# Performance work log

Hardware: AMD Instinct MI355X
Metric: run time of the kernel (lower is better)

## Reference

```python
import jax, jax.numpy as jnp
import numpy as np

B, T, H, L = 128, 256, 512, 2  # batch, seq_len, hidden(=input), num_layers


def setup_inputs() -> dict:
    key = jax.random.key(0)
    k0, k1, k2, k3 = jax.random.split(key, 4)
    s = 1.0 / np.sqrt(H)  # torch Linear default init range
    x = jax.random.normal(k0, (B, T, H), jnp.float32)
    # Gate order along last dim: [i, f, g, o]; axis 1 = direction (0=fwd, 1=bwd)
    Wx = jax.random.uniform(k1, (L, 2, H, 4 * H), jnp.float32, -s, s)  # input->gates (W_ii,W_if,W_ig,W_io)
    Wh = jax.random.uniform(k2, (L, 2, H, 4 * H), jnp.float32, -s, s)  # hidden->gates (no bias)
    b = jax.random.uniform(k3, (L, 2, 4 * H), jnp.float32, -s, s)      # input-projection biases
    return {"x": x, "Wx": Wx, "Wh": Wh, "b": b}


def _lstm_scan(xproj, Wh_ld):
    # xproj: [T, B, 4H] precomputed input projection; Wh_ld: [H, 4H]
    Hh = Wh_ld.shape[0]
    bsz = xproj.shape[1]
    h0 = jnp.zeros((bsz, Hh), xproj.dtype)
    c0 = jnp.zeros((bsz, Hh), xproj.dtype)

    def step(carry, xp):
        h, c = carry
        gates = xp + h @ Wh_ld  # [B, 4H]
        i = jax.nn.sigmoid(gates[:, :Hh])
        f = jax.nn.sigmoid(gates[:, Hh:2 * Hh])
        g = jnp.tanh(gates[:, 2 * Hh:3 * Hh])
        o = jax.nn.sigmoid(gates[:, 3 * Hh:])
        c_new = f * c + i * g
        h_new = o * jnp.tanh(c_new)
        return (h_new, c_new), h_new

    _, hs = jax.lax.scan(step, (h0, c0), xproj)
    return hs  # [T, B, H]


def _run_direction(x, Wx, Wh, b, d):
    # x: [B, T, in]; d=0 forward, d=1 backward (time-reversed)
    nl = Wx.shape[0]
    seq = jnp.flip(x, axis=1) if d == 1 else x
    inp = seq
    for l in range(nl):
        # batched input projection over all timesteps (one big GEMM)
        xproj = jnp.einsum('bti,ig->btg', inp, Wx[l, d]) + b[l, d]  # [B, T, 4H]
        hs = _lstm_scan(jnp.transpose(xproj, (1, 0, 2)), Wh[l, d])   # [T, B, H]
        inp = jnp.transpose(hs, (1, 0, 2))  # [B, T, H]
        # dropout between layers is identity at inference
    return jnp.flip(inp, axis=1) if d == 1 else inp


def reference(x, Wx, Wh, b):
    fwd = _run_direction(x, Wx, Wh, b, 0)
    bwd = _run_direction(x, Wx, Wh, b, 1)
    return jnp.concatenate([fwd, bwd], axis=-1)  # [B, T, 2H]
```

## Files before the change

kernel.cpp:

```cpp
#include <hip/hip_runtime.h>

typedef unsigned short ushort_t;
typedef unsigned int u32;
typedef unsigned long long u64;
typedef __attribute__((ext_vector_type(8))) short short8;
typedef __attribute__((ext_vector_type(4))) float floatx4;

#define Tt 256
#define Hh 512
#define NBLK 256
#define THREADS 512
#define RWS 64
#define PING_ELEMS 65536u
#define KCH 256
#define SLOT_SHORTS (RWS * KCH)
#define SMEM_BYTES (2*SLOT_SHORTS*2 + RWS*16*2 + RWS*16*4)

__device__ __forceinline__ float sigf(float x)  { return 1.0f / (1.0f + __expf(-x)); }
__device__ __forceinline__ float tanhf_(float x){ return 1.0f - 2.0f / (__expf(2.0f*x) + 1.0f); }

__device__ __forceinline__ ushort_t f2bf(float f) {
  u32 u = __float_as_uint(f);
  u += 0x7FFFu + ((u >> 16) & 1u);
  return (ushort_t)(u >> 16);
}

__device__ __forceinline__ u64 pload(const ushort_t* p) {
  return __hip_atomic_load((const u64*)p, __ATOMIC_RELAXED, __HIP_MEMORY_SCOPE_AGENT);
}
__device__ __forceinline__ void pstore(ushort_t* p, u64 v) {
  __hip_atomic_store((u64*)p, v, __ATOMIC_RELAXED, __HIP_MEMORY_SCOPE_AGENT);
}
__device__ __forceinline__ u32 aload32(const u32* p) {
  return __hip_atomic_load(p, __ATOMIC_RELAXED, __HIP_MEMORY_SCOPE_AGENT);
}
__device__ __forceinline__ void astore32(u32* p, u32 v) {
  __hip_atomic_store(p, v, __ATOMIC_RELAXED, __HIP_MEMORY_SCOPE_AGENT);
}

__device__ __forceinline__ void gridbar(u32* gen, u32* flags, int fi, bool agg,
                                        u32 target) {
  __syncthreads();
  const int tid = threadIdx.x;
  if (agg) {
    if (tid < 64) {
      if (tid == 0) {
        asm volatile("s_waitcnt vmcnt(0)" ::: "memory");
        astore32(flags + fi * 16, target);
      }
      for (;;) {
        u32 a = aload32(flags + tid * 16);
        u32 b = aload32(flags + (tid + 64) * 16);
        if (__all((int)(a >= target && b >= target))) break;
        __builtin_amdgcn_s_sleep(1);
      }
      if (tid == 0) astore32(gen, target);
    }
  } else if (tid == 0) {
    asm volatile("s_waitcnt vmcnt(0)" ::: "memory");
    astore32(flags + fi * 16, target);
    while (aload32(gen) < target) __builtin_amdgcn_s_sleep(1);
  }
  asm volatile("" ::: "memory");
  __syncthreads();
}

__global__ __launch_bounds__(THREADS, 2) void bilstm_scan(
    const float* __restrict__ x,
    const float* __restrict__ Wx,
    const float* __restrict__ Wh,
    const float* __restrict__ bias,
    ushort_t* __restrict__ ping,
    u32* __restrict__ barws,
    float* __restrict__ out)
{
  extern __shared__ __align__(16) char smem[];
  short* actb = (short*)smem;
  ushort_t* hrep = (ushort_t*)(smem + 2 * SLOT_SHORTS * 2);
  float* hrep32 = (float*)(smem + 2 * SLOT_SHORTS * 2 + RWS*16*2);

  const int blk = blockIdx.x;
  const int cb = blk & 31, nb = (blk >> 5) & 1, l = (blk >> 6) & 1, d = blk >> 7;
  const int rb0 = nb * RWS;
  const int fi = blk & 127;
  const bool agg = (fi == 0);
  const int tid = threadIdx.x;
  const int wvi = tid >> 6, lane = tid & 63;
  const int mw = wvi & 3, nw = wvi >> 2;
  const int q = lane >> 4, ln = lane & 15;
  const int rl = tid >> 3, et = tid & 7;
  const int rot = (rl >> 1) & 31;
  u32* gen = barws + d * 16;
  u32* flags = barws + 64 + d * 2048;

  for (int i = tid; i < (int)(SMEM_BYTES / 4); i += THREADS) ((u32*)smem)[i] = 0u;
  __syncthreads();

  short8 wreg[32];
  {
    const float* wxb = Wx + (size_t)(l * 2 + d) * 512 * 2048;
    const float* whb = Wh + (size_t)(l * 2 + d) * 512 * 2048;
    const int col = (ln & 3) * 512 + cb * 16 + mw * 4 + (ln >> 2);
#pragma unroll
    for (int kc = 0; kc < 32; ++kc) {
      union { short8 v; ushort_t u[8]; } tmp;
#pragma unroll
      for (int j2 = 0; j2 < 8; ++j2) {
        const int k = kc * 32 + q * 8 + j2;
        const float wv_ = (k < 512) ? wxb[(size_t)k * 2048 + col]
                                    : whb[(size_t)(k - 512) * 2048 + col];
        tmp.u[j2] = f2bf(wv_);
      }
      wreg[kc] = tmp.v;
    }
  }

  float brs[4];
  {
    const float* bp = bias + (size_t)(l * 2 + d) * 2048;
    const int j = cb * 16 + mw * 4 + q;
#pragma unroll
    for (int r = 0; r < 4; ++r) brs[r] = bp[r * 512 + j];
  }

  float cst[2];
  cst[0] = 0.f; cst[1] = 0.f;

  const size_t own_base = (size_t)(l ? 4 : 0) + d * 2;

  for (int it = 0; it <= Tt; ++it) {
    const bool active = (l == 0) ? (it < Tt) : (it >= 1);
    if (active) {
      const int t = (l == 0) ? it : (it - 1);

      const float* xf = nullptr;
      const ushort_t* xh = nullptr;
      if (l == 0) {
        const int tx = d ? (Tt - 1 - t) : t;
        xf = x + (size_t)tx * Hh;
      } else {
        xh = ping + (size_t)(d * 2 + ((t + 1) & 1)) * PING_ELEMS;
      }
      const ushort_t* hp = ping + (own_base + (t & 1)) * PING_ELEMS;
      ushort_t* hdst = ping + (own_base + ((t + 1) & 1)) * PING_ELEMS;

      floatx4 acc[2];
      {
        floatx4 z4 = {0.f, 0.f, 0.f, 0.f};
        acc[0] = z4; acc[1] = z4;
      }

      u64 gA[4][2], gB[4][2];

      auto h_issue = [&](const ushort_t* base, int kcol, u64 (&g)[4][2]) {
        const ushort_t* s = base + (size_t)(rb0 + rl) * Hh + kcol + et * 32;
#pragma unroll
        for (int uu = 0; uu < 4; ++uu) {
          g[uu][0] = pload(s + uu * 8);
          g[uu][1] = pload(s + uu * 8 + 4);
        }
      };
      auto h_commit = [&](int kc, u64 (&g)[4][2]) {
        short* dst = actb + (kc & 1) * SLOT_SHORTS;
#pragma unroll
        for (int uu = 0; uu < 4; ++uu) {
          uint4 v;
          v.x = (u32)g[uu][0]; v.y = (u32)(g[uu][0] >> 32);
          v.z = (u32)g[uu][1]; v.w = (u32)(g[uu][1] >> 32);
          const int pos = (et * 4 + uu + rot) & 31;
          *(uint4*)&dst[rl * KCH + pos * 8] = v;
        }
      };
      auto x_stage = [&](int kc) {
        short* dst = actb + (kc & 1) * SLOT_SHORTS;
        const float* s = xf + (size_t)(rb0 + rl) * ((size_t)Tt * Hh) + kc * KCH + et * 32;
#pragma unroll
        for (int uu = 0; uu < 4; ++uu) {
          floatx4 f0 = *(const floatx4*)(s + uu * 8);
          floatx4 f1 = *(const floatx4*)(s + uu * 8 + 4);
          union { uint4 v; ushort_t us[8]; } pk;
#pragma unroll
          for (int e = 0; e < 4; ++e) {
            pk.us[e] = f2bf(f0[e]);
            pk.us[4 + e] = f2bf(f1[e]);
          }
          const int pos = (et * 4 + uu + rot) & 31;
          *(uint4*)&dst[rl * KCH + pos * 8] = pk.v;
        }
      };

      auto compute = [&](int kc) {
        const short* src = actb + (kc & 1) * SLOT_SHORTS;
#pragma unroll
        for (int s = 0; s < 8; ++s) {
          short8 af[2];
#pragma unroll
          for (int nt = 0; nt < 2; ++nt) {
            const int b = nw * 32 + nt * 16 + ln;
            const int pos = (s * 4 + q + ((b >> 1) & 31)) & 31;
            af[nt] = *(const short8*)&src[b * KCH + pos * 8];
          }
          const int kidx = kc * 8 + s;
#pragma unroll
          for (int nt = 0; nt < 2; ++nt)
            acc[nt] = __builtin_amdgcn_mfma_f32_16x16x32_bf16(
                wreg[kidx], af[nt], acc[nt], 0, 0, 0);
        }
      };

      if (l == 0) {
        h_issue(hp, 0, gA);
        h_issue(hp, 256, gB);
        x_stage(0);
        __syncthreads();
        x_stage(1);
        compute(0);
        __syncthreads();
        h_commit(2, gA);
        compute(1);
        __syncthreads();
        h_commit(3, gB);
        compute(2);
        __syncthreads();
        compute(3);
      } else {
        h_issue(xh, 0, gA);
        h_issue(xh, 256, gB);
        h_commit(0, gA);
        __syncthreads();
        h_commit(1, gB);
        h_issue(hp, 0, gA);
        compute(0);
        __syncthreads();
        h_commit(2, gA);
        h_issue(hp, 256, gB);
        compute(1);
        __syncthreads();
        h_commit(3, gB);
        compute(2);
        __syncthreads();
        compute(3);
      }

      const int tout = d ? (Tt - 1 - t) : t;
      const int jj = mw * 4 + q;
#pragma unroll
      for (int nt = 0; nt < 2; ++nt) {
        const int b = nw * 32 + nt * 16 + ln;
        float iv = sigf  (acc[nt][0] + brs[0]);
        float fv = sigf  (acc[nt][1] + brs[1]);
        float gv = tanhf_(acc[nt][2] + brs[2]);
        float ov = sigf  (acc[nt][3] + brs[3]);
        float cv = fv * cst[nt] + iv * gv;
        cst[nt] = cv;
        float hv = ov * tanhf_(cv);
        hrep[b * 16 + jj] = f2bf(hv);
        if (l == 1) hrep32[b * 16 + jj] = hv;
      }
      __syncthreads();
      if (tid < 256) {
        const int rr = tid >> 2, qt = tid & 3;
        u64 hv64 = *(const u64*)&hrep[rr * 16 + qt * 4];
        ushort_t* dp = hdst + (size_t)(rb0 + rr) * Hh + cb * 16 + qt * 4;
        pstore(dp, hv64);
        if (l == 1) {
          float* op = out + ((size_t)(rb0 + rr) * Tt + tout) * 1024 + d * 512 + cb * 16 + qt * 4;
          *(floatx4*)op = *(const floatx4*)&hrep32[rr * 16 + qt * 4];
        }
      }
    }
    gridbar(gen, flags, fi, agg, (u32)it + 1u);
  }
}

extern "C" void kernel_launch(void* const* d_in, const int* in_sizes, int n_in,
                              void* d_out, int out_size, void* d_ws, size_t ws_size,
                              hipStream_t stream) {
  const float* x    = (const float*)d_in[0];
  const float* Wx   = (const float*)d_in[1];
  const float* Wh   = (const float*)d_in[2];
  const float* bias = (const float*)d_in[3];

  u32* bar = (u32*)d_ws;
  ushort_t* ping = (ushort_t*)((char*)d_ws + 32768);

  hipFuncSetAttribute((const void*)bilstm_scan,
                      hipFuncAttributeMaxDynamicSharedMemorySize, SMEM_BYTES);

  hipMemsetAsync(d_ws, 0, 32768 + (size_t)8 * PING_ELEMS * sizeof(ushort_t), stream);

  hipLaunchKernelGGL(bilstm_scan, dim3(NBLK), dim3(THREADS), SMEM_BYTES, stream,
                     x, Wx, Wh, bias, ping, bar, (float*)d_out);
}
```

Before: 3.950 ms.

## Decentralize grid barrier and prestage next-step inputs before the barrier

The grid barrier drops the aggregator-and-generation scheme: every block now polls all 128 per-block flags directly, which removes one hop of latency per step. The input half of the next timestep (layer 0: the x slice; layer 1: the layer-0 h output) is staged into shared memory before the barrier, so only the recurrent h half is loaded after it. To support this, the layer-1 lag grows to two steps and layer 0 keeps a four-deep ring of h buffers, which enlarges the workspace. The cost is more polling traffic from every block and one extra iteration.

```diff
diff --git a/kernel.cpp b/kernel.cpp
--- a/kernel.cpp
+++ b/kernel.cpp
@@ -11,6 +11,7 @@
 #define NBLK 256
 #define THREADS 512
 #define RWS 64
+#define NIT 258
 #define PING_ELEMS 65536u
 #define KCH 256
 #define SLOT_SHORTS (RWS * KCH)
@@ -38,28 +39,20 @@
   __hip_atomic_store(p, v, __ATOMIC_RELAXED, __HIP_MEMORY_SCOPE_AGENT);
 }
 
-__device__ __forceinline__ void gridbar(u32* gen, u32* flags, int fi, bool agg,
-                                        u32 target) {
+__device__ __forceinline__ void gridbar(u32* flags, int fi, u32 target) {
   __syncthreads();
   const int tid = threadIdx.x;
-  if (agg) {
-    if (tid < 64) {
-      if (tid == 0) {
-        asm volatile("s_waitcnt vmcnt(0)" ::: "memory");
-        astore32(flags + fi * 16, target);
-      }
-      for (;;) {
-        u32 a = aload32(flags + tid * 16);
-        u32 b = aload32(flags + (tid + 64) * 16);
-        if (__all((int)(a >= target && b >= target))) break;
-        __builtin_amdgcn_s_sleep(1);
-      }
-      if (tid == 0) astore32(gen, target);
-    }
-  } else if (tid == 0) {
+  if (tid == 0) {
     asm volatile("s_waitcnt vmcnt(0)" ::: "memory");
     astore32(flags + fi * 16, target);
-    while (aload32(gen) < target) __builtin_amdgcn_s_sleep(1);
+  }
+  if (tid < 64) {
+    for (;;) {
+      u32 a = aload32(flags + tid * 16);
+      u32 b = aload32(flags + (tid + 64) * 16);
+      if (__all((int)(a >= target && b >= target))) break;
+      __builtin_amdgcn_s_sleep(1);
+    }
   }
   asm volatile("" ::: "memory");
   __syncthreads();
@@ -83,15 +76,14 @@
   const int cb = blk & 31, nb = (blk >> 5) & 1, l = (blk >> 6) & 1, d = blk >> 7;
   const int rb0 = nb * RWS;
   const int fi = blk & 127;
-  const bool agg = (fi == 0);
   const int tid = threadIdx.x;
   const int wvi = tid >> 6, lane = tid & 63;
   const int mw = wvi & 3, nw = wvi >> 2;
   const int q = lane >> 4, ln = lane & 15;
   const int rl = tid >> 3, et = tid & 7;
   const int rot = (rl >> 1) & 31;
-  u32* gen = barws + d * 16;
   u32* flags = barws + 64 + d * 2048;
+  ushort_t* dbase = ping + (size_t)d * 6 * PING_ELEMS;
 
   for (int i = tid; i < (int)(SMEM_BYTES / 4); i += THREADS) ((u32*)smem)[i] = 0u;
   __syncthreads();
@@ -126,23 +118,67 @@
   float cst[2];
   cst[0] = 0.f; cst[1] = 0.f;
 
-  const size_t own_base = (size_t)(l ? 4 : 0) + d * 2;
-
-  for (int it = 0; it <= Tt; ++it) {
-    const bool active = (l == 0) ? (it < Tt) : (it >= 1);
+  auto x_prestage = [&](int tn) {
+    const int tx = d ? (Tt - 1 - tn) : tn;
+    const float* xf = x + (size_t)tx * Hh;
+#pragma unroll
+    for (int kc = 0; kc < 2; ++kc) {
+      short* dst = actb + kc * SLOT_SHORTS;
+      const float* s = xf + (size_t)(rb0 + rl) * ((size_t)Tt * Hh) + kc * KCH + et * 32;
+#pragma unroll
+      for (int uu = 0; uu < 4; ++uu) {
+        floatx4 f0 = *(const floatx4*)(s + uu * 8);
+        floatx4 f1 = *(const floatx4*)(s + uu * 8 + 4);
+        union { uint4 v; ushort_t us[8]; } pk;
+#pragma unroll
+        for (int e = 0; e < 4; ++e) {
+          pk.us[e] = f2bf(f0[e]);
+          pk.us[4 + e] = f2bf(f1[e]);
+        }
+        const int pos = (et * 4 + uu + rot) & 31;
+        *(uint4*)&dst[rl * KCH + pos * 8] = pk.v;
+      }
+    }
+  };
+
+  auto h0_prestage = [&](int tn) {
+    const ushort_t* h0 = dbase + (size_t)(tn & 3) * PING_ELEMS;
+    const ushort_t* s = h0 + (size_t)(rb0 + rl) * Hh + et * 32;
+    u64 g[8][2];
+#pragma unroll
+    for (int c = 0; c < 2; ++c)
+#pragma unroll
+      for (int uu = 0; uu < 4; ++uu) {
+        g[c * 4 + uu][0] = pload(s + c * 256 + uu * 8);
+        g[c * 4 + uu][1] = pload(s + c * 256 + uu * 8 + 4);
+      }
+#pragma unroll
+    for (int c = 0; c < 2; ++c) {
+      short* dst = actb + c * SLOT_SHORTS;
+#pragma unroll
+      for (int uu = 0; uu < 4; ++uu) {
+        uint4 v;
+        v.x = (u32)g[c * 4 + uu][0]; v.y = (u32)(g[c * 4 + uu][0] >> 32);
+        v.z = (u32)g[c * 4 + uu][1]; v.w = (u32)(g[c * 4 + uu][1] >> 32);
+        const int pos = (et * 4 + uu + rot) & 31;
+        *(uint4*)&dst[rl * KCH + pos * 8] = v;
+      }
+    }
+  };
+
+  if (l == 0) x_prestage(0);
+
+  for (int it = 0; it < NIT; ++it) {
+    const bool active = (l == 0) ? (it < Tt) : (it >= 2);
+    const int t = (l == 0) ? it : (it - 2);
+
     if (active) {
-      const int t = (l == 0) ? it : (it - 1);
-
-      const float* xf = nullptr;
-      const ushort_t* xh = nullptr;
-      if (l == 0) {
-        const int tx = d ? (Tt - 1 - t) : t;
-        xf = x + (size_t)tx * Hh;
-      } else {
-        xh = ping + (size_t)(d * 2 + ((t + 1) & 1)) * PING_ELEMS;
-      }
-      const ushort_t* hp = ping + (own_base + (t & 1)) * PING_ELEMS;
-      ushort_t* hdst = ping + (own_base + ((t + 1) & 1)) * PING_ELEMS;
+      const ushort_t* hp = (l == 0)
+          ? dbase + (size_t)((t + 3) & 3) * PING_ELEMS
+          : dbase + (size_t)(4 + (t & 1)) * PING_ELEMS;
+      ushort_t* hdst = (l == 0)
+          ? dbase + (size_t)(t & 3) * PING_ELEMS
+          : dbase + (size_t)(4 + ((t + 1) & 1)) * PING_ELEMS;
 
       floatx4 acc[2];
       {
@@ -151,9 +187,8 @@
       }
 
       u64 gA[4][2], gB[4][2];
-
-      auto h_issue = [&](const ushort_t* base, int kcol, u64 (&g)[4][2]) {
-        const ushort_t* s = base + (size_t)(rb0 + rl) * Hh + kcol + et * 32;
+      auto h_issue = [&](int kcol, u64 (&g)[4][2]) {
+        const ushort_t* s = hp + (size_t)(rb0 + rl) * Hh + kcol + et * 32;
 #pragma unroll
         for (int uu = 0; uu < 4; ++uu) {
           g[uu][0] = pload(s + uu * 8);
@@ -171,24 +206,6 @@
           *(uint4*)&dst[rl * KCH + pos * 8] = v;
         }
       };
-      auto x_stage = [&](int kc) {
-        short* dst = actb + (kc & 1) * SLOT_SHORTS;
-        const float* s = xf + (size_t)(rb0 + rl) * ((size_t)Tt * Hh) + kc * KCH + et * 32;
-#pragma unroll
-        for (int uu = 0; uu < 4; ++uu) {
-          floatx4 f0 = *(const floatx4*)(s + uu * 8);
-          floatx4 f1 = *(const floatx4*)(s + uu * 8 + 4);
-          union { uint4 v; ushort_t us[8]; } pk;
-#pragma unroll
-          for (int e = 0; e < 4; ++e) {
-            pk.us[e] = f2bf(f0[e]);
-            pk.us[4 + e] = f2bf(f1[e]);
-          }
-          const int pos = (et * 4 + uu + rot) & 31;
-          *(uint4*)&dst[rl * KCH + pos * 8] = pk.v;
-        }
-      };
-
       auto compute = [&](int kc) {
         const short* src = actb + (kc & 1) * SLOT_SHORTS;
 #pragma unroll
@@ -208,39 +225,17 @@
         }
       };
 
-      if (l == 0) {
-        h_issue(hp, 0, gA);
-        h_issue(hp, 256, gB);
-        x_stage(0);
-        __syncthreads();
-        x_stage(1);
-        compute(0);
-        __syncthreads();
-        h_commit(2, gA);
-        compute(1);
-        __syncthreads();
-        h_commit(3, gB);
-        compute(2);
-        __syncthreads();
-        compute(3);
-      } else {
-        h_issue(xh, 0, gA);
-        h_issue(xh, 256, gB);
-        h_commit(0, gA);
-        __syncthreads();
-        h_commit(1, gB);
-        h_issue(hp, 0, gA);
-        compute(0);
-        __syncthreads();
-        h_commit(2, gA);
-        h_issue(hp, 256, gB);
-        compute(1);
-        __syncthreads();
-        h_commit(3, gB);
-        compute(2);
-        __syncthreads();
-        compute(3);
-      }
+      h_issue(0, gA);
+      h_issue(256, gB);
+      compute(0);
+      __syncthreads();
+      h_commit(2, gA);
+      compute(1);
+      __syncthreads();
+      h_commit(3, gB);
+      compute(2);
+      __syncthreads();
+      compute(3);
 
       const int tout = d ? (Tt - 1 - t) : t;
       const int jj = mw * 4 + q;
@@ -269,7 +264,14 @@
         }
       }
     }
-    gridbar(gen, flags, fi, agg, (u32)it + 1u);
+
+    const bool nact = (l == 0) ? (it + 1 < Tt) : (it + 1 >= 2 && it + 1 < NIT);
+    if (nact) {
+      if (l == 0) x_prestage(it + 1);
+      else        h0_prestage(it - 1);
+    }
+
+    gridbar(flags, fi, (u32)it + 1u);
   }
 }
 
@@ -287,7 +289,7 @@
   hipFuncSetAttribute((const void*)bilstm_scan,
                       hipFuncAttributeMaxDynamicSharedMemorySize, SMEM_BYTES);
 
-  hipMemsetAsync(d_ws, 0, 32768 + (size_t)8 * PING_ELEMS * sizeof(ushort_t), stream);
+  hipMemsetAsync(d_ws, 0, 32768 + (size_t)12 * PING_ELEMS * sizeof(ushort_t), stream);
 
   hipLaunchKernelGGL(bilstm_scan, dim3(NBLK), dim3(THREADS), SMEM_BYTES, stream,
                      x, Wx, Wh, bias, ping, bar, (float*)d_out);
```

Result: faster. 3.813 ms (-3.5%).
